# Performance work log

Hardware: AMD Instinct MI355X
Metric: run time of the kernel (lower is better)

Reference implementation:

```python
import jax, jax.numpy as jnp
import numpy as np

EMBED_DIM = 1024
CONTEXT_LEN = 2048
NUM_HEADS = 16
HEAD_DIM = EMBED_DIM // NUM_HEADS
BATCH = 2
SEQ = 2048


def setup_inputs() -> dict:
    key = jax.random.key(0)
    ks = jax.random.split(key, 6)
    s = 1.0 / np.sqrt(EMBED_DIM)
    x = jax.random.normal(ks[0], (BATCH, SEQ, EMBED_DIM), dtype=jnp.float32)
    # nn.Linear weights stored as [out, in]; we keep [in, out] for x @ W
    W_q = jax.random.uniform(ks[1], (EMBED_DIM, EMBED_DIM), jnp.float32, -s, s)
    W_k = jax.random.uniform(ks[2], (EMBED_DIM, EMBED_DIM), jnp.float32, -s, s)
    W_v = jax.random.uniform(ks[3], (EMBED_DIM, EMBED_DIM), jnp.float32, -s, s)
    W_o = jax.random.uniform(ks[4], (EMBED_DIM, EMBED_DIM), jnp.float32, -s, s)
    b_o = jax.random.uniform(ks[5], (EMBED_DIM,), jnp.float32, -s, s)
    return {"x": x, "W_q": W_q, "W_k": W_k, "W_v": W_v, "W_o": W_o, "b_o": b_o}


def reference(x, W_q, W_k, W_v, W_o, b_o):
    b, s, _ = x.shape
    # project and split heads: [b, s, e] -> [b, h, s, d]
    def heads(t):
        return t.reshape(b, s, NUM_HEADS, HEAD_DIM).transpose(0, 2, 1, 3)
    q = heads(x @ W_q)
    k = heads(x @ W_k)
    v = heads(x @ W_v)
    scores = jnp.einsum("bhqd,bhkd->bhqk", q, k)  # full seq x seq scores
    causal = jnp.triu(jnp.ones((s, s), dtype=bool), k=1)
    scores = jnp.where(causal, -jnp.inf, scores)
    attn = jax.nn.softmax(scores / np.sqrt(HEAD_DIM).astype(np.float32), axis=-1)
    ctx = jnp.einsum("bhqk,bhkd->bhqd", attn, v)
    ctx = ctx.transpose(0, 2, 1, 3).reshape(b, s, EMBED_DIM)
    return ctx @ W_o + b_o
```

## Files before the change

kernel.cpp:

```cpp
#include <hip/hip_runtime.h>

#define EMBED 1024
#define SEQL  2048
#define NHEAD 16
#define HDIM  64
#define NBATCH 2
#define MROWS 4096

typedef __attribute__((ext_vector_type(4))) float  f32x4;
typedef __attribute__((ext_vector_type(8))) __bf16 bf16x8;

__device__ __forceinline__ short f2bf(float f){
  __bf16 h = (__bf16)f;
  union { __bf16 h; short s; } u; u.h = h;
  return u.s;
}

#define GLDS(gp, lp) __builtin_amdgcn_global_load_lds( \
    (const __attribute__((address_space(1))) void*)(gp), \
    (__attribute__((address_space(3))) void*)(lp), 16, 0, 0)

#define WAITV(N) do { asm volatile("s_waitcnt vmcnt(" #N ")" ::: "memory"); \
                      __builtin_amdgcn_sched_barrier(0); } while(0)
#define BARRIER() do { __builtin_amdgcn_s_barrier(); \
                       __builtin_amdgcn_sched_barrier(0); } while(0)

__global__ __launch_bounds__(256) void prep_kernel(const float* __restrict__ x,
    const float* __restrict__ W0, const float* __restrict__ W1,
    const float* __restrict__ W2, const float* __restrict__ W3,
    short* __restrict__ Xb, short* __restrict__ WtAll){
  const int z = blockIdx.z;
  if (z < 4){
    __shared__ float T[64][65];
    const int idx = blockIdx.y*32 + blockIdx.x;
    if (idx >= 256) return;
    const float* W = (z==0)?W0:(z==1)?W1:(z==2)?W2:W3;
    short* Wt = WtAll + z*(EMBED*EMBED);
    const int bx = (idx & 15)*64;
    const int by = (idx >> 4)*64;
    const int c4 = (threadIdx.x & 15)*4;
    const int tr = threadIdx.x >> 4;
    #pragma unroll
    for (int i=0;i<4;++i){
      int r = 16*i + tr;
      float4 v = *(const float4*)(W + (by + r)*EMBED + bx + c4);
      T[c4+0][r] = v.x; T[c4+1][r] = v.y; T[c4+2][r] = v.z; T[c4+3][r] = v.w;
    }
    __syncthreads();
    #pragma unroll
    for (int i=0;i<4;++i){
      int n = 16*i + tr;
      short4 o;
      o.x = f2bf(T[n][c4+0]); o.y = f2bf(T[n][c4+1]);
      o.z = f2bf(T[n][c4+2]); o.w = f2bf(T[n][c4+3]);
      *(short4*)(Wt + (bx + n)*EMBED + by + c4) = o;
    }
  } else {
    const int blk = (z-4)*1024 + blockIdx.y*32 + blockIdx.x;
    const int i = (blk*256 + threadIdx.x)*4;
    float4 v = *(const float4*)(x + i);
    short4 o; o.x=f2bf(v.x); o.y=f2bf(v.y); o.z=f2bf(v.z); o.w=f2bf(v.w);
    *(short4*)(Xb + i) = o;
  }
}

__global__ __launch_bounds__(512, 2) void gemm_qkv_kernel(const short* __restrict__ Xb,
    const short* __restrict__ WtAll, short* __restrict__ Q, short* __restrict__ K,
    short* __restrict__ Vt){
  __shared__ __align__(16) short SH[65536];
  const int tid  = threadIdx.x;
  const int lane = tid & 63;
  const int wid  = tid >> 6;
  const int wm   = wid >> 2;
  const int wn   = wid & 3;
  const int l15  = lane & 15, lg = lane >> 4;
  const int swzS = (l15 & 7) << 3;
  const int m0 = blockIdx.x * 256;
  const int n0 = blockIdx.y * 256;
  const int z  = blockIdx.z;
  const short* A  = Xb;
  const short* Bt = WtAll + z*(EMBED*EMBED);

  f32x4 acc[8][4] = {};

  auto STAGEH = [&](int mat, int h, int t){
    const short* src  = mat ? Bt : A;
    const int   base0 = mat ? n0 : m0;
    short* dst = SH + (t&1)*32768 + mat*16384 + h*8192;
    #pragma unroll
    for (int g=0; g<2; ++g){
      int c = g*512 + tid;
      int r = c >> 3;
      int p = (c & 7) ^ (r & 7);
      GLDS(src + (base0 + 128*h + r)*1024 + t*64 + p*8, dst + c*8);
    }
  };

  auto PH = [&](int t, int qm, int qn){
    const short* As = SH + (t&1)*32768;
    const short* Bs = As + 16384;
    bf16x8 a[4][2], b[2][2];
    #pragma unroll
    for (int i=0;i<4;++i){
      int row = qm*128 + wm*64 + 16*i + l15;
      #pragma unroll
      for (int kh=0;kh<2;++kh)
        a[i][kh] = *(const bf16x8*)(As + row*64 + ((kh*32 + 8*lg) ^ swzS));
    }
    #pragma unroll
    for (int j=0;j<2;++j){
      int row = qn*128 + wn*32 + 16*j + l15;
      #pragma unroll
      for (int kh=0;kh<2;++kh)
        b[j][kh] = *(const bf16x8*)(Bs + row*64 + ((kh*32 + 8*lg) ^ swzS));
    }
    BARRIER();
    __builtin_amdgcn_s_setprio(1);
    #pragma unroll
    for (int i=0;i<4;++i)
      #pragma unroll
      for (int j=0;j<2;++j)
        #pragma unroll
        for (int kh=0;kh<2;++kh)
          acc[qm*4+i][qn*2+j] = __builtin_amdgcn_mfma_f32_16x16x32_bf16(
              a[i][kh], b[j][kh], acc[qm*4+i][qn*2+j], 0,0,0);
    __builtin_amdgcn_s_setprio(0);
    WAITV(6);
    BARRIER();
  };

  STAGEH(0,0,0); STAGEH(1,0,0); STAGEH(1,1,0); STAGEH(0,1,0);
  STAGEH(0,0,1); STAGEH(1,0,1);
  WAITV(4);
  BARRIER();

  for (int t = 0; t < 16; ++t){
    if (t+1 < 16) STAGEH(1,1,t+1);
    PH(t, 0, 0);
    if (t+1 < 16) STAGEH(0,1,t+1);
    PH(t, 1, 0);
    if (t+2 < 16) STAGEH(1,0,t+2);
    PH(t, 0, 1);
    if (t+2 < 16) STAGEH(0,0,t+2);
    PH(t, 1, 1);
  }
  WAITV(0);
  __syncthreads();

  const int bb = m0 >> 11, srow0 = m0 & 2047;
  if (z < 2){
    short* out = z ? K : Q;
    const float qscl = (z==0) ? (0.125f * 1.44269504f) : 1.0f;
    #pragma unroll
    for (int mi=0; mi<8; ++mi)
      #pragma unroll
      for (int nj=0; nj<4; ++nj)
        #pragma unroll
        for (int rr=0; rr<4; ++rr){
          int m = m0 + 128*(mi>>2) + 64*wm + 16*(mi&3) + 4*lg + rr;
          int n = n0 + 128*(nj>>1) + 32*wn + 16*(nj&1) + l15;
          int srow = m & 2047, hh = n >> 6, d = n & 63;
          out[(((bb<<4)+hh)*SEQL + srow)*HDIM + d] = f2bf(acc[mi][nj][rr] * qscl);
        }
  } else {
    short* T = SH;
    #pragma unroll
    for (int mi=0; mi<8; ++mi)
      #pragma unroll
      for (int nj=0; nj<4; ++nj){
        int n_loc = 128*(nj>>1) + 32*wn + 16*(nj&1) + l15;
        int mb    = 128*(mi>>2) + 64*wm + 16*(mi&3) + 4*lg;
        short4 pk;
        pk.x = f2bf(acc[mi][nj][0]); pk.y = f2bf(acc[mi][nj][1]);
        pk.z = f2bf(acc[mi][nj][2]); pk.w = f2bf(acc[mi][nj][3]);
        *(short4*)(T + n_loc*256 + (mb ^ ((n_loc & 7) << 3))) = pk;
      }
    __syncthreads();
    #pragma unroll
    for (int it=0; it<16; ++it){
      int ci    = it*512 + tid;
      int n_loc = ci >> 5;
      int mch   = (ci & 31) * 8;
      int4 v = *(const int4*)(T + n_loc*256 + (mch ^ ((n_loc & 7) << 3)));
      int n_glob = n0 + n_loc;
      int hh = n_glob >> 6, d = n_glob & 63;
      *(int4*)(Vt + (((bb<<4)+hh)*HDIM + d)*SEQL + srow0 + mch) = v;
    }
  }
}

__device__ __forceinline__ void gemm_tile_64(const short* __restrict__ A,
    const short* __restrict__ Bt, short* As, short* Bs, int m0, int n0, f32x4 acc[2][4]){
  const int tid  = threadIdx.x;
  const int lane = tid & 63;
  const int wid  = tid >> 6;
  const int wrow = (wid >> 1) * 32, wcol = (wid & 1) * 64;
  const int arow = tid >> 2, acol8 = (tid & 3) * 8;
  const int l15 = lane & 15, lg = lane >> 4;

  auto STAGE = [&](int b, int k0){
    short* as = As + b*2048;
    short* bs = Bs + b*4096;
    GLDS(A  + (m0      + arow) * 1024 + k0 + acol8, as + tid*8);
    GLDS(Bt + (n0      + arow) * 1024 + k0 + acol8, bs + tid*8);
    GLDS(Bt + (n0 + 64 + arow) * 1024 + k0 + acol8, bs + 2048 + tid*8);
  };

  auto KSTEP = [&](int b){
    const short* as = As + b*2048;
    const short* bs = Bs + b*4096;
    bf16x8 a[2], bb[4];
    #pragma unroll
    for (int i=0;i<2;++i) a[i]  = *(const bf16x8*)(as + (wrow+16*i+l15)*32 + 8*lg);
    #pragma unroll
    for (int j=0;j<4;++j) bb[j] = *(const bf16x8*)(bs + (wcol+16*j+l15)*32 + 8*lg);
    #pragma unroll
    for (int i=0;i<2;++i)
      #pragma unroll
      for (int j=0;j<4;++j)
        acc[i][j] = __builtin_amdgcn_mfma_f32_16x16x32_bf16(a[i], bb[j], acc[i][j], 0,0,0);
  };

  STAGE(0, 0); STAGE(1, 32);
  __syncthreads();
  for (int p = 0; p < 16; ++p){
    const int k0 = p*64;
    if (p + 1 < 16){ STAGE((2*p+2)&3, k0+64); STAGE((2*p+3)&3, k0+96); }
    KSTEP((2*p)&3);
    KSTEP((2*p+1)&3);
    __syncthreads();
  }
}

__global__ __launch_bounds__(256) void gemm_out_kernel(const short* __restrict__ Ctx,
    const short* __restrict__ WtO, const float* __restrict__ bias, float* __restrict__ out){
  __shared__ __align__(16) short As[4*2048], Bs[4*4096];
  const int m0 = blockIdx.x*64, n0 = blockIdx.y*128;
  f32x4 acc[2][4] = {};
  gemm_tile_64(Ctx, WtO, As, Bs, m0, n0, acc);
  const int lane = threadIdx.x & 63;
  const int wid  = threadIdx.x >> 6;
  const int wrow = (wid >> 1) * 32, wcol = (wid & 1) * 64;
  const int l15 = lane & 15, lg = lane >> 4;
  #pragma unroll
  for (int i=0;i<2;++i)
    #pragma unroll
    for (int j=0;j<4;++j)
      #pragma unroll
      for (int r=0;r<4;++r){
        int m = m0 + wrow + 16*i + 4*lg + r;
        int n = n0 + wcol + 16*j + l15;
        out[m*EMBED + n] = acc[i][j][r] + bias[n];
      }
}

__global__ __launch_bounds__(512, 4) void attn_kernel(const short* __restrict__ Q,
    const short* __restrict__ K, const short* __restrict__ Vt, short* __restrict__ Ctx){
  __shared__ __align__(16) char lds[81920];
  const int tid  = threadIdx.x;
  const int lane = tid & 63;
  const int wid  = tid >> 6;
  const int bid   = blockIdx.x;
  const int xcd   = bid & 7;
  const int i7    = bid >> 3;
  const int bh    = xcd + 8*(i7 & 3);
  const int cidx  = i7 >> 2;
  const int chunk = (cidx < 8) ? cidx : 23 - cidx;
  const int q0blk = chunk * 128;
  const int ntp   = chunk + 1;
  const int q0w   = q0blk + 16*wid;
  const int qlast = q0w + 15;

  const short* Qh  = Q  + bh*(SEQL*HDIM);
  const char*  KhB = (const char*)(K  + bh*(SEQL*HDIM));
  const char*  VhB = (const char*)(Vt + bh*(HDIM*SEQL));
  const int l15 = lane & 15, lg = lane >> 4;
  const int lg20 = 20 * lg;
  const int swE = (l15 & 7) << 3;
  const int swB = (l15 & 7) << 4;
  const int laneRow = lane >> 3;
  const int colSwz  = 16 * ((lane & 7) ^ laneRow);
  const int r0 = 8 * wid;

  const short* qp = Qh + (q0w + l15)*HDIM + 8*lg;
  bf16x8 bq0 = *(const bf16x8*)qp;
  bf16x8 bq1 = *(const bf16x8*)(qp + 32);

  f32x4 acc[4];
  #pragma unroll
  for (int j=0; j<4; ++j) acc[j] = (f32x4){0.f,0.f,0.f,0.f};
  float mrun = -3e30f, lrun = 0.f;

  short* pw = (short*)(lds + 65536 + wid*2048);

  auto STAGE = [&](int b, int t){
    char* kb = lds + b*16384;
    char* vb = kb + 8192;
    const int kv0 = t*64;
    GLDS(KhB + (kv0 + r0 + laneRow)*128 + colSwz, kb + r0*128);
    GLDS(VhB + (r0 + laneRow)*4096 + kv0*2 + colSwz, vb + r0*128);
  };

  auto QKHALF = [&](const char* kb, f32x4 sc[4]){
    #pragma unroll
    for (int c=0; c<4; ++c){
      const char* kr = kb + (16*c + l15)*128;
      bf16x8 k0 = *(const bf16x8*)(kr + ((16*lg) ^ swB));
      bf16x8 k1 = *(const bf16x8*)(kr + ((64 + 16*lg) ^ swB));
      f32x4 zz = (f32x4){0.f,0.f,0.f,0.f};
      zz = __builtin_amdgcn_mfma_f32_16x16x32_bf16(k0, bq0, zz, 0,0,0);
      zz = __builtin_amdgcn_mfma_f32_16x16x32_bf16(k1, bq1, zz, 0,0,0);
      sc[c] = zz;
    }
  };

  STAGE(0, 0); STAGE(1, 1);
  __syncthreads();

  for (int tp = 0; tp < ntp; ++tp){
    const int t0   = 2*tp;
    const int kv00 = t0*64;
    const int kv01 = kv00 + 64;
    if (tp + 1 < ntp){ STAGE((t0+2)&3, t0+2); STAGE((t0+3)&3, t0+3); }
    if (kv00 <= qlast){
      const char* kb0 = lds + (t0&3)*16384;
      const char* kb1 = lds + ((t0+1)&3)*16384;
      const bool  h1  = (kv01 <= qlast);
      f32x4 sc0[4], sc1[4];
      __builtin_amdgcn_s_setprio(1);
      QKHALF(kb0, sc0);
      if (h1) QKHALF(kb1, sc1);
      __builtin_amdgcn_s_setprio(0);
      if (kv00 + 63 > q0w){
        #pragma unroll
        for (int c=0; c<4; ++c)
          #pragma unroll
          for (int r=0; r<4; ++r)
            if (kv00 + 16*c + 4*lg + r > q0w + l15) sc0[c][r] = -3e30f;
      }
      if (h1 && kv01 + 63 > q0w){
        #pragma unroll
        for (int c=0; c<4; ++c)
          #pragma unroll
          for (int r=0; r<4; ++r)
            if (kv01 + 16*c + 4*lg + r > q0w + l15) sc1[c][r] = -3e30f;
      }
      float cm[4];
      #pragma unroll
      for (int c=0; c<4; ++c)
        cm[c] = fmaxf(fmaxf(sc0[c][0], sc0[c][1]), fmaxf(sc0[c][2], sc0[c][3]));
      float pm = fmaxf(fmaxf(cm[0], cm[1]), fmaxf(cm[2], cm[3]));
      if (h1){
        float dm[4];
        #pragma unroll
        for (int c=0; c<4; ++c)
          dm[c] = fmaxf(fmaxf(sc1[c][0], sc1[c][1]), fmaxf(sc1[c][2], sc1[c][3]));
        pm = fmaxf(pm, fmaxf(fmaxf(dm[0], dm[1]), fmaxf(dm[2], dm[3])));
      }
      pm = fmaxf(pm, __shfl_xor(pm, 16));
      pm = fmaxf(pm, __shfl_xor(pm, 32));
      const int resc = !__all(pm <= mrun);
      float mn = mrun, ss = 1.0f;
      if (resc){
        mn = fmaxf(mrun, pm);
        ss = __builtin_amdgcn_exp2f(mrun - mn);
        mrun = mn;
      }
      #pragma unroll
      for (int c=0; c<4; ++c)
        #pragma unroll
        for (int r=0; r<4; ++r)
          sc0[c][r] = __builtin_amdgcn_exp2f(sc0[c][r] - mn);
      float cs[4];
      #pragma unroll
      for (int c=0; c<4; ++c)
        cs[c] = (sc0[c][0] + sc0[c][1]) + (sc0[c][2] + sc0[c][3]);
      float ls = (cs[0] + cs[1]) + (cs[2] + cs[3]);
      if (h1){
        #pragma unroll
        for (int c=0; c<4; ++c)
          #pragma unroll
          for (int r=0; r<4; ++r)
            sc1[c][r] = __builtin_amdgcn_exp2f(sc1[c][r] - mn);
        float ds[4];
        #pragma unroll
        for (int c=0; c<4; ++c)
          ds[c] = (sc1[c][0] + sc1[c][1]) + (sc1[c][2] + sc1[c][3]);
        ls += (ds[0] + ds[1]) + (ds[2] + ds[3]);
      }
      ls += __shfl_xor(ls, 16);
      ls += __shfl_xor(ls, 32);
      if (resc){
        lrun = lrun*ss + ls;
        float srg[4];
        #pragma unroll
        for (int r=0; r<4; ++r) srg[r] = __shfl(ss, lg20 + r);
        #pragma unroll
        for (int j=0; j<4; ++j)
          #pragma unroll
          for (int r=0; r<4; ++r) acc[j][r] *= srg[r];
      } else {
        lrun += ls;
      }
      #pragma unroll
      for (int c=0; c<4; ++c){
        short4 pk;
        pk.x = f2bf(sc0[c][0]); pk.y = f2bf(sc0[c][1]);
        pk.z = f2bf(sc0[c][2]); pk.w = f2bf(sc0[c][3]);
        *(short4*)(pw + l15*64 + ((16*c + 4*lg) ^ swE)) = pk;
      }
      {
        bf16x8 pa0 = *(const bf16x8*)(pw + l15*64 + ((8*lg)      ^ swE));
        bf16x8 pa1 = *(const bf16x8*)(pw + l15*64 + ((32 + 8*lg) ^ swE));
        const char* vb = kb0 + 8192;
        __builtin_amdgcn_s_setprio(1);
        #pragma unroll
        for (int j=0; j<4; ++j){
          const char* vrp = vb + (16*j + l15)*128;
          bf16x8 v0 = *(const bf16x8*)(vrp + ((16*lg) ^ swB));
          bf16x8 v1 = *(const bf16x8*)(vrp + ((64 + 16*lg) ^ swB));
          acc[j] = __builtin_amdgcn_mfma_f32_16x16x32_bf16(pa0, v0, acc[j], 0,0,0);
          acc[j] = __builtin_amdgcn_mfma_f32_16x16x32_bf16(pa1, v1, acc[j], 0,0,0);
        }
        __builtin_amdgcn_s_setprio(0);
      }
      if (h1){
        #pragma unroll
        for (int c=0; c<4; ++c){
          short4 pk;
          pk.x = f2bf(sc1[c][0]); pk.y = f2bf(sc1[c][1]);
          pk.z = f2bf(sc1[c][2]); pk.w = f2bf(sc1[c][3]);
          *(short4*)(pw + l15*64 + ((16*c + 4*lg) ^ swE)) = pk;
        }
        bf16x8 pa0 = *(const bf16x8*)(pw + l15*64 + ((8*lg)      ^ swE));
        bf16x8 pa1 = *(const bf16x8*)(pw + l15*64 + ((32 + 8*lg) ^ swE));
        const char* vb = kb1 + 8192;
        __builtin_amdgcn_s_setprio(1);
        #pragma unroll
        for (int j=0; j<4; ++j){
          const char* vrp = vb + (16*j + l15)*128;
          bf16x8 v0 = *(const bf16x8*)(vrp + ((16*lg) ^ swB));
          bf16x8 v1 = *(const bf16x8*)(vrp + ((64 + 16*lg) ^ swB));
          acc[j] = __builtin_amdgcn_mfma_f32_16x16x32_bf16(pa0, v0, acc[j], 0,0,0);
          acc[j] = __builtin_amdgcn_mfma_f32_16x16x32_bf16(pa1, v1, acc[j], 0,0,0);
        }
        __builtin_amdgcn_s_setprio(0);
      }
    }
    __syncthreads();
  }

  const int bb = bh >> 4, hh = bh & 15;
  float lr[4];
  #pragma unroll
  for (int r=0; r<4; ++r) lr[r] = __builtin_amdgcn_rcpf(__shfl(lrun, lg20 + r));
  #pragma unroll
  for (int j=0; j<4; ++j)
    #pragma unroll
    for (int r=0; r<4; ++r){
      int qg = q0w + 4*lg + r;
      Ctx[(bb*SEQL + qg)*EMBED + hh*HDIM + 16*j + l15] = f2bf(acc[j][r] * lr[r]);
    }
}

extern "C" void kernel_launch(void* const* d_in, const int* in_sizes, int n_in,
                              void* d_out, int out_size, void* d_ws, size_t ws_size,
                              hipStream_t stream){
  const float* x  = (const float*)d_in[0];
  const float* Wq = (const float*)d_in[1];
  const float* Wk = (const float*)d_in[2];
  const float* Wv = (const float*)d_in[3];
  const float* Wo = (const float*)d_in[4];
  const float* bo = (const float*)d_in[5];
  float* out = (float*)d_out;

  char* ws = (char*)d_ws;
  const size_t MB = 1u << 20;
  short* Xb  = (short*)(ws +  0*MB);
  short* Wt  = (short*)(ws +  8*MB);
  short* Q   = (short*)(ws + 16*MB);
  short* Kk  = (short*)(ws + 24*MB);
  short* Vt  = (short*)(ws + 32*MB);
  short* Ctx = (short*)(ws + 40*MB);

  prep_kernel<<<dim3(32,32,8), 256, 0, stream>>>(x, Wq, Wk, Wv, Wo, Xb, Wt);
  gemm_qkv_kernel<<<dim3(16,4,3), 512, 0, stream>>>(Xb, Wt, Q, Kk, Vt);
  attn_kernel<<<512, 512, 0, stream>>>(Q, Kk, Vt, Ctx);
  gemm_out_kernel<<<dim3(64,8), 256, 0, stream>>>(Ctx, Wt + 3*(EMBED*EMBED), bo, out);
}
```

Baseline: 104.2 us.

## Restructure QKV GEMM into three-stage K=32 pipeline with larger warp tiles

Replaces the double-buffered K=64 half-tile staging with a triple-buffered ring of K=32 slices. Each warp now owns a contiguous 128x64 sub-tile, so every slice feeds 32 MFMAs. This cuts shared memory from 128KB to 96KB so two blocks fit per CU, and allows a simpler prefetch-two-ahead schedule. The V transpose epilogue is split into two halves so it fits in the smaller buffer, which adds extra barriers. The risks are more barriers per unit of K, since each iteration now covers half as much K, and higher register pressure from holding 8+4 fragments at once.

```diff
diff --git a/kernel.cpp b/kernel.cpp
--- a/kernel.cpp
+++ b/kernel.cpp
@@ -67,14 +67,13 @@
 __global__ __launch_bounds__(512, 2) void gemm_qkv_kernel(const short* __restrict__ Xb,
     const short* __restrict__ WtAll, short* __restrict__ Q, short* __restrict__ K,
     short* __restrict__ Vt){
-  __shared__ __align__(16) short SH[65536];
+  __shared__ __align__(16) short SH[49152];
   const int tid  = threadIdx.x;
   const int lane = tid & 63;
   const int wid  = tid >> 6;
   const int wm   = wid >> 2;
   const int wn   = wid & 3;
   const int l15  = lane & 15, lg = lane >> 4;
-  const int swzS = (l15 & 7) << 3;
   const int m0 = blockIdx.x * 256;
   const int n0 = blockIdx.y * 256;
   const int z  = blockIdx.z;
@@ -83,68 +82,58 @@
 
   f32x4 acc[8][4] = {};
 
-  auto STAGEH = [&](int mat, int h, int t){
-    const short* src  = mat ? Bt : A;
-    const int   base0 = mat ? n0 : m0;
-    short* dst = SH + (t&1)*32768 + mat*16384 + h*8192;
-    #pragma unroll
-    for (int g=0; g<2; ++g){
-      int c = g*512 + tid;
-      int r = c >> 3;
-      int p = (c & 7) ^ (r & 7);
-      GLDS(src + (base0 + 128*h + r)*1024 + t*64 + p*8, dst + c*8);
-    }
-  };
-
-  auto PH = [&](int t, int qm, int qn){
-    const short* As = SH + (t&1)*32768;
-    const short* Bs = As + 16384;
-    bf16x8 a[4][2], b[2][2];
-    #pragma unroll
-    for (int i=0;i<4;++i){
-      int row = qm*128 + wm*64 + 16*i + l15;
-      #pragma unroll
-      for (int kh=0;kh<2;++kh)
-        a[i][kh] = *(const bf16x8*)(As + row*64 + ((kh*32 + 8*lg) ^ swzS));
-    }
-    #pragma unroll
-    for (int j=0;j<2;++j){
-      int row = qn*128 + wn*32 + 16*j + l15;
-      #pragma unroll
-      for (int kh=0;kh<2;++kh)
-        b[j][kh] = *(const bf16x8*)(Bs + row*64 + ((kh*32 + 8*lg) ^ swzS));
+  const int sr = tid >> 2;
+  const int sc = tid & 3;
+  const int sp = sc ^ (sr & 3);
+
+  auto STAGE_T = [&](int t){
+    short* slot = SH + (t%3)*16384;
+    #pragma unroll
+    for (int mat=0; mat<2; ++mat){
+      const short* src  = mat ? Bt : A;
+      const int   base0 = mat ? n0 : m0;
+      #pragma unroll
+      for (int h=0; h<2; ++h)
+        GLDS(src + (base0 + 128*h + sr)*1024 + t*32 + sp*8,
+             slot + mat*8192 + h*4096 + tid*8);
+    }
+  };
+
+  auto PHASE = [&](int t){
+    const short* As = SH + (t%3)*16384;
+    const short* Bs = As + 8192;
+    bf16x8 a[8], b[4];
+    #pragma unroll
+    for (int i=0;i<8;++i){
+      int row = wm*128 + 16*i + l15;
+      a[i] = *(const bf16x8*)(As + row*32 + ((8*lg) ^ ((row&3)<<3)));
+    }
+    #pragma unroll
+    for (int j=0;j<4;++j){
+      int row = wn*64 + 16*j + l15;
+      b[j] = *(const bf16x8*)(Bs + row*32 + ((8*lg) ^ ((row&3)<<3)));
     }
     BARRIER();
     __builtin_amdgcn_s_setprio(1);
     #pragma unroll
-    for (int i=0;i<4;++i)
-      #pragma unroll
-      for (int j=0;j<2;++j)
-        #pragma unroll
-        for (int kh=0;kh<2;++kh)
-          acc[qm*4+i][qn*2+j] = __builtin_amdgcn_mfma_f32_16x16x32_bf16(
-              a[i][kh], b[j][kh], acc[qm*4+i][qn*2+j], 0,0,0);
+    for (int i=0;i<8;++i)
+      #pragma unroll
+      for (int j=0;j<4;++j)
+        acc[i][j] = __builtin_amdgcn_mfma_f32_16x16x32_bf16(a[i], b[j], acc[i][j], 0,0,0);
     __builtin_amdgcn_s_setprio(0);
-    WAITV(6);
-    BARRIER();
-  };
-
-  STAGEH(0,0,0); STAGEH(1,0,0); STAGEH(1,1,0); STAGEH(0,1,0);
-  STAGEH(0,0,1); STAGEH(1,0,1);
+  };
+
+  STAGE_T(0); STAGE_T(1);
   WAITV(4);
   BARRIER();
 
-  for (int t = 0; t < 16; ++t){
-    if (t+1 < 16) STAGEH(1,1,t+1);
-    PH(t, 0, 0);
-    if (t+1 < 16) STAGEH(0,1,t+1);
-    PH(t, 1, 0);
-    if (t+2 < 16) STAGEH(1,0,t+2);
-    PH(t, 0, 1);
-    if (t+2 < 16) STAGEH(0,0,t+2);
-    PH(t, 1, 1);
+  for (int t = 0; t < 32; ++t){
+    if (t + 2 < 32) STAGE_T(t+2);
+    PHASE(t);
+    if (t + 2 < 32) { WAITV(4); }
+    else            { WAITV(0); }
+    BARRIER();
   }
-  WAITV(0);
   __syncthreads();
 
   const int bb = m0 >> 11, srow0 = m0 & 2047;
@@ -157,34 +146,40 @@
       for (int nj=0; nj<4; ++nj)
         #pragma unroll
         for (int rr=0; rr<4; ++rr){
-          int m = m0 + 128*(mi>>2) + 64*wm + 16*(mi&3) + 4*lg + rr;
-          int n = n0 + 128*(nj>>1) + 32*wn + 16*(nj&1) + l15;
+          int m = m0 + wm*128 + 16*mi + 4*lg + rr;
+          int n = n0 + wn*64 + 16*nj + l15;
           int srow = m & 2047, hh = n >> 6, d = n & 63;
           out[(((bb<<4)+hh)*SEQL + srow)*HDIM + d] = f2bf(acc[mi][nj][rr] * qscl);
         }
   } else {
     short* T = SH;
     #pragma unroll
-    for (int mi=0; mi<8; ++mi)
-      #pragma unroll
-      for (int nj=0; nj<4; ++nj){
-        int n_loc = 128*(nj>>1) + 32*wn + 16*(nj&1) + l15;
-        int mb    = 128*(mi>>2) + 64*wm + 16*(mi&3) + 4*lg;
-        short4 pk;
-        pk.x = f2bf(acc[mi][nj][0]); pk.y = f2bf(acc[mi][nj][1]);
-        pk.z = f2bf(acc[mi][nj][2]); pk.w = f2bf(acc[mi][nj][3]);
-        *(short4*)(T + n_loc*256 + (mb ^ ((n_loc & 7) << 3))) = pk;
-      }
-    __syncthreads();
-    #pragma unroll
-    for (int it=0; it<16; ++it){
-      int ci    = it*512 + tid;
-      int n_loc = ci >> 5;
-      int mch   = (ci & 31) * 8;
-      int4 v = *(const int4*)(T + n_loc*256 + (mch ^ ((n_loc & 7) << 3)));
-      int n_glob = n0 + n_loc;
-      int hh = n_glob >> 6, d = n_glob & 63;
-      *(int4*)(Vt + (((bb<<4)+hh)*HDIM + d)*SEQL + srow0 + mch) = v;
+    for (int h=0; h<2; ++h){
+      if ((wn >> 1) == h){
+        #pragma unroll
+        for (int mi=0; mi<8; ++mi)
+          #pragma unroll
+          for (int nj=0; nj<4; ++nj){
+            int n_loc = (wn & 1)*64 + 16*nj + l15;
+            int mb    = wm*128 + 16*mi + 4*lg;
+            short4 pk;
+            pk.x = f2bf(acc[mi][nj][0]); pk.y = f2bf(acc[mi][nj][1]);
+            pk.z = f2bf(acc[mi][nj][2]); pk.w = f2bf(acc[mi][nj][3]);
+            *(short4*)(T + n_loc*256 + (mb ^ ((n_loc & 7) << 3))) = pk;
+          }
+      }
+      __syncthreads();
+      #pragma unroll
+      for (int it=0; it<8; ++it){
+        int ci    = it*512 + tid;
+        int n_loc = ci >> 5;
+        int mch   = (ci & 31) * 8;
+        int4 v = *(const int4*)(T + n_loc*256 + (mch ^ ((n_loc & 7) << 3)));
+        int n_glob = n0 + h*128 + n_loc;
+        int hh = n_glob >> 6, d = n_glob & 63;
+        *(int4*)(Vt + (((bb<<4)+hh)*HDIM + d)*SEQL + srow0 + mch) = v;
+      }
+      __syncthreads();
     }
   }
 }
```

Result: no change. 105.4 us (+1.2%).
